# Kernel tuning notes

Hardware: AMD Instinct MI355X
Metric: run time of the kernel (lower is better)

Reference implementation:

```python
import jax, jax.numpy as jnp
import numpy as np

NUM_HEADS = 16
D_MODEL = 1024
D_K = D_MODEL // NUM_HEADS


def setup_inputs() -> dict:
    key = jax.random.key(0)
    ks = jax.random.split(key, 12)
    B, S = 2, 2048
    scale = 1.0 / np.sqrt(D_MODEL)
    inp = {
        "query": jax.random.normal(ks[0], (B, S, D_MODEL), jnp.float32),
        "key": jax.random.normal(ks[1], (B, S, D_MODEL), jnp.float32),
        "value": jax.random.normal(ks[2], (B, S, D_MODEL), jnp.float32),
        "mask": jnp.ones((B, S, S), jnp.int32),
        "Wq": jax.random.normal(ks[3], (D_MODEL, D_MODEL), jnp.float32) * scale,
        "bq": jax.random.normal(ks[4], (D_MODEL,), jnp.float32) * scale,
        "Wk": jax.random.normal(ks[5], (D_MODEL, D_MODEL), jnp.float32) * scale,
        "bk": jax.random.normal(ks[6], (D_MODEL,), jnp.float32) * scale,
        "Wv": jax.random.normal(ks[7], (D_MODEL, D_MODEL), jnp.float32) * scale,
        "bv": jax.random.normal(ks[8], (D_MODEL,), jnp.float32) * scale,
        "Wo": jax.random.normal(ks[9], (D_MODEL, D_MODEL), jnp.float32) * scale,
        "bo": jax.random.normal(ks[10], (D_MODEL,), jnp.float32) * scale,
    }
    return inp


def _split_heads(x):
    B, S, _ = x.shape
    return x.reshape(B, S, NUM_HEADS, D_K).transpose(0, 2, 1, 3)  # [B,H,S,d_k]


def reference(query, key, value, mask, Wq, bq, Wk, bk, Wv, bv, Wo, bo):
    # torch Linear: y = x @ W.T + b
    q = _split_heads(query @ Wq.T + bq)
    k = _split_heads(key @ Wk.T + bk)
    v = _split_heads(value @ Wv.T + bv)
    scores = jnp.einsum("bhqd,bhkd->bhqk", q, k) / np.sqrt(D_K)
    scores = jnp.where(mask[:, None, :, :] == 0, jnp.float32(-1e9), scores)
    p_attn = jax.nn.softmax(scores, axis=-1)
    attn = jnp.einsum("bhqk,bhkd->bhqd", p_attn, v)  # [B,H,S,d_k]
    B, _, S, _ = attn.shape
    x = attn.transpose(0, 2, 1, 3).reshape(B, S, D_MODEL)
    return x @ Wo.T + bo
```

## Files before the change

kernel.cpp:

```cpp
#include <hip/hip_runtime.h>
#include <hip/hip_bf16.h>
#include <cstdint>

#define DEVINL static __device__ __forceinline__

typedef __attribute__((ext_vector_type(4))) float floatx4;
typedef __attribute__((ext_vector_type(8))) short bf16x8;

DEVINL unsigned short f2bf(float f) {
    union { float f; uint32_t u; } v; v.f = f;
    return (unsigned short)((v.u + 0x7FFFu + ((v.u >> 16) & 1u)) >> 16);
}

DEVINL uint32_t pk2bf(float x, float y) {
    __hip_bfloat162 h = __float22bfloat162_rn(float2{x, y});
    union { __hip_bfloat162 h; uint32_t u; } v; v.h = h;
    return v.u;
}

DEVINL floatx4 mfma16(bf16x8 a, bf16x8 b, floatx4 c) {
    return __builtin_amdgcn_mfma_f32_16x16x32_bf16(a, b, c, 0, 0, 0);
}

#define GLDS16(g, l)                                                            \
    __builtin_amdgcn_global_load_lds(                                           \
        (const __attribute__((address_space(1))) void*)(g),                     \
        (__attribute__((address_space(3))) void*)(l), 16, 0, 0)

constexpr int B_ = 2, S_ = 2048, D_ = 1024, H_ = 16, DK_ = 64;
constexpr int BSROWS = B_ * S_;
constexpr int NQB = S_ / 128;
constexpr int NKT = S_ / 64;

constexpr float QSCALE = 0.18033688011112042f;

__device__ int g_flags[B_ * NQB * NKT];

__global__ __launch_bounds__(256, 2)
void gemm_qkv(const float* __restrict__ q, const float* __restrict__ k,
              const float* __restrict__ v,
              const float* __restrict__ Wq, const float* __restrict__ Wk,
              const float* __restrict__ Wv,
              const float* __restrict__ bq, const float* __restrict__ bk,
              const float* __restrict__ bv,
              const int* __restrict__ mask,
              unsigned short* __restrict__ Qp, unsigned short* __restrict__ KpF,
              unsigned short* __restrict__ VpF)
{
    constexpr int K = D_, N = D_;
    __shared__ unsigned short As[2][128 * 64];
    __shared__ unsigned short Bs[2][128 * 64];
    __shared__ int fflag;

    const int bid = blockIdx.x;

    if (bid < 1024) {
        int mb = bid;
        int kt = mb & 31, qq = (mb >> 5) & 15, b = mb >> 9;
        const int* base = mask + (size_t)(b * S_ + qq * 128) * S_ + kt * 64;
        int ok = 1;
        #pragma unroll
        for (int i = 0; i < 8; ++i) {
            int u = threadIdx.x + 256 * i;
            int row = u >> 4, c = u & 15;
            int4 m = *(const int4*)(base + (size_t)row * S_ + c * 4);
            if ((m.x == 0) | (m.y == 0) | (m.z == 0) | (m.w == 0)) ok = 0;
        }
        if (threadIdx.x == 0) fflag = 1;
        __syncthreads();
        if (!ok) fflag = 0;
        __syncthreads();
        if (threadIdx.x == 0) g_flags[mb] = fflag;
        return;
    }

    const int gb = bid - 1024;
    const int xcd = gb & 7, sl = gb >> 3;
    const int z = sl >> 5, rr = sl & 31;
    const int nb = rr >> 2, mloc = rr & 3;
    const int m0 = (mloc * 8 + xcd) * 128, n0 = nb * 128;

    const float* A    = z == 0 ? q  : z == 1 ? k  : v;
    const float* W    = z == 0 ? Wq : z == 1 ? Wk : Wv;
    const float* bias = z == 0 ? bq : z == 1 ? bk : bv;

    const int tid  = threadIdx.x;
    const int lane = tid & 63, wave = tid >> 6;
    const int lr = lane & 15, lg = lane >> 4;
    const int wm = (wave >> 1) * 64, wn = (wave & 1) * 64;

    int rowA[4], kcA[4];
    #pragma unroll
    for (int j = 0; j < 4; ++j) {
        int L = (wave * 4 + j) * 64 + lane;
        rowA[j] = L >> 3; kcA[j] = (L & 7) ^ (rowA[j] & 7);
    }

    float4 ra[4][2], rw[4][2];
    auto loadStage = [&](int k0) {
        #pragma unroll
        for (int j = 0; j < 4; ++j) {
            const float* pa = A + (size_t)(m0 + rowA[j]) * K + k0 + kcA[j] * 8;
            ra[j][0] = *(const float4*)pa;
            ra[j][1] = *(const float4*)(pa + 4);
            const float* pw = W + (size_t)(n0 + rowA[j]) * K + k0 + kcA[j] * 8;
            rw[j][0] = *(const float4*)pw;
            rw[j][1] = *(const float4*)(pw + 4);
        }
    };
    auto writeStage = [&](int buf) {
        #pragma unroll
        for (int j = 0; j < 4; ++j) {
            uint4 o;
            o.x = pk2bf(ra[j][0].x, ra[j][0].y); o.y = pk2bf(ra[j][0].z, ra[j][0].w);
            o.z = pk2bf(ra[j][1].x, ra[j][1].y); o.w = pk2bf(ra[j][1].z, ra[j][1].w);
            *(uint4*)&As[buf][(wave * 4 + j) * 512 + lane * 8] = o;
            uint4 p;
            p.x = pk2bf(rw[j][0].x, rw[j][0].y); p.y = pk2bf(rw[j][0].z, rw[j][0].w);
            p.z = pk2bf(rw[j][1].x, rw[j][1].y); p.w = pk2bf(rw[j][1].z, rw[j][1].w);
            *(uint4*)&Bs[buf][(wave * 4 + j) * 512 + lane * 8] = p;
        }
    };

    floatx4 acc[4][4];
    #pragma unroll
    for (int mt = 0; mt < 4; ++mt)
        #pragma unroll
        for (int nt = 0; nt < 4; ++nt)
            acc[mt][nt] = floatx4{0.f, 0.f, 0.f, 0.f};

    loadStage(0);
    writeStage(0);
    __syncthreads();
    for (int it = 0; it < K / 64; ++it) {
        const int buf = it & 1;
        if (it + 1 < K / 64) loadStage((it + 1) * 64);

        #pragma unroll
        for (int kf = 0; kf < 2; ++kf) {
            bf16x8 af[4], bfr[4];
            #pragma unroll
            for (int mt = 0; mt < 4; ++mt) {
                int row = wm + mt * 16 + lr;
                af[mt] = *(const bf16x8*)&As[buf][row * 64 + (((kf * 4 + lg) ^ (lr & 7)) * 8)];
            }
            #pragma unroll
            for (int nt = 0; nt < 4; ++nt) {
                int row = wn + nt * 16 + lr;
                bfr[nt] = *(const bf16x8*)&Bs[buf][row * 64 + (((kf * 4 + lg) ^ (lr & 7)) * 8)];
            }
            #pragma unroll
            for (int mt = 0; mt < 4; ++mt)
                #pragma unroll
                for (int nt = 0; nt < 4; ++nt)
                    acc[mt][nt] = mfma16(af[mt], bfr[nt], acc[mt][nt]);
        }

        if (it + 1 < K / 64) writeStage(buf ^ 1);
        __syncthreads();
    }

    if (z == 0) {
        #pragma unroll
        for (int nt = 0; nt < 4; ++nt) {
            int col = n0 + wn + nt * 16 + lr;
            float bv2 = bias[col];
            #pragma unroll
            for (int mt = 0; mt < 4; ++mt)
                #pragma unroll
                for (int reg = 0; reg < 4; ++reg) {
                    int row = m0 + wm + mt * 16 + lg * 4 + reg;
                    Qp[(size_t)row * N + col] = f2bf((acc[mt][nt][reg] + bv2) * QSCALE);
                }
        }
    } else if (z == 1) {
        #pragma unroll
        for (int nt = 0; nt < 4; ++nt) {
            int c = n0 + wn + nt * 16 + lr;
            int h = c >> 6, d = c & 63;
            int kfA = d >> 5, lgA = (d >> 3) & 3, j = d & 7;
            float bv2 = bias[c];
            #pragma unroll
            for (int mt = 0; mt < 4; ++mt)
                #pragma unroll
                for (int reg = 0; reg < 4; ++reg) {
                    int t = m0 + wm + mt * 16 + lg * 4 + reg;
                    int bb = t >> 11, sx = t & (S_ - 1);
                    int kt = sx >> 6, key = sx & 63;
                    int mtA = key >> 4, lrA = key & 15;
                    size_t off = (((size_t)(bb * 16 + h) * 32 + kt) * 8 + (kfA * 4 + mtA)) * 512
                               + (lrA + 16 * lgA) * 8 + j;
                    KpF[off] = f2bf(acc[mt][nt][reg] + bv2);
                }
        }
    } else {
        #pragma unroll
        for (int nt = 0; nt < 4; ++nt) {
            int c = n0 + wn + nt * 16 + lr;
            int h = c >> 6, dtA = (c >> 4) & 3;
            float bv2 = bias[c];
            #pragma unroll
            for (int mt = 0; mt < 4; ++mt) {
                int t0 = m0 + wm + mt * 16 + lg * 4;
                int bb = t0 >> 11, s0 = t0 & (S_ - 1);
                int kt = s0 >> 6, key = s0 & 63;
                int kfA = key >> 5, lgA = (key >> 3) & 3, j0 = key & 7;
                size_t off = (((size_t)(bb * 16 + h) * 32 + kt) * 8 + (dtA * 2 + kfA)) * 512
                           + (lr + 16 * lgA) * 8 + j0;
                uint2 p;
                p.x = pk2bf(acc[mt][nt][0] + bv2, acc[mt][nt][1] + bv2);
                p.y = pk2bf(acc[mt][nt][2] + bv2, acc[mt][nt][3] + bv2);
                *(uint2*)&VpF[off] = p;
            }
        }
    }
}

__global__ __launch_bounds__(256, 2)
void attn_flash(const unsigned short* __restrict__ Qp,
                const unsigned short* __restrict__ KpF,
                const unsigned short* __restrict__ VpF,
                const int* __restrict__ mask,
                unsigned short* __restrict__ Out)
{
    constexpr int LD = 72;
    __shared__ unsigned short Ps[128 * LD];

    const int tid = threadIdx.x;
    const int lane = tid & 63, wave = tid >> 6;
    const int lr = lane & 15, lg = lane >> 4;
    const int id = blockIdx.x;
    const int hb = id & 31;
    const int h = hb & 15, b = hb >> 4;
    const int qb = ((id >> 8) << 3) | ((id >> 5) & 7);
    const int q0 = qb * 128, qw = q0 + wave * 32;

    bf16x8 qf[2][2];
    #pragma unroll
    for (int qt = 0; qt < 2; ++qt)
        #pragma unroll
        for (int kf = 0; kf < 2; ++kf)
            qf[qt][kf] = *(const bf16x8*)(Qp + (size_t)(b * S_ + qw + qt * 16 + lr) * D_ +
                                          h * DK_ + kf * 32 + lg * 8);

    float l_[2] = {0.f, 0.f};
    floatx4 o_acc[2][4];
    #pragma unroll
    for (int qt = 0; qt < 2; ++qt)
        #pragma unroll
        for (int dt = 0; dt < 4; ++dt) o_acc[qt][dt] = floatx4{0.f, 0.f, 0.f, 0.f};

    const unsigned short* kbase = KpF + (size_t)(b * 16 + h) * 32 * 4096 + lane * 8;
    const unsigned short* vbase = VpF + (size_t)(b * 16 + h) * 32 * 4096 + lane * 8;
    const int fbase = (b * NQB + qb) * NKT;
    unsigned short* PsW = &Ps[(wave * 32 + lr) * LD];

    auto loadKV = [&](int kt, bf16x8 (&kfr)[8], bf16x8 (&vfr)[8]) {
        const unsigned short* kb = kbase + kt * 4096;
        const unsigned short* vb = vbase + kt * 4096;
        #pragma unroll
        for (int c = 0; c < 8; ++c) kfr[c] = *(const bf16x8*)(kb + c * 512);
        #pragma unroll
        for (int c = 0; c < 8; ++c) vfr[c] = *(const bf16x8*)(vb + c * 512);
    };

    auto process = [&](int kt, bf16x8 (&kfr)[8], bf16x8 (&vfr)[8]) {
        floatx4 sc[2][4];
        #pragma unroll
        for (int qt = 0; qt < 2; ++qt)
            #pragma unroll
            for (int mt = 0; mt < 4; ++mt) sc[qt][mt] = floatx4{0.f, 0.f, 0.f, 0.f};
        #pragma unroll
        for (int mt = 0; mt < 4; ++mt)
            #pragma unroll
            for (int kf = 0; kf < 2; ++kf)
                #pragma unroll
                for (int qt = 0; qt < 2; ++qt)
                    sc[qt][mt] = mfma16(kfr[kf * 4 + mt], qf[qt][kf], sc[qt][mt]);

        if (g_flags[fbase + kt] == 0) {
            #pragma unroll
            for (int qt = 0; qt < 2; ++qt) {
                int qq = qw + qt * 16 + lr;
                const int* mrow = mask + (size_t)(b * S_ + qq) * S_ + kt * 64;
                #pragma unroll
                for (int mt = 0; mt < 4; ++mt)
                    #pragma unroll
                    for (int reg = 0; reg < 4; ++reg)
                        if (mrow[mt * 16 + lg * 4 + reg] == 0)
                            sc[qt][mt][reg] = -1e9f;
            }
        }

        #pragma unroll
        for (int qt = 0; qt < 2; ++qt) {
            #pragma unroll
            for (int mt = 0; mt < 4; ++mt) {
                float p0 = __builtin_amdgcn_exp2f(sc[qt][mt][0]);
                float p1 = __builtin_amdgcn_exp2f(sc[qt][mt][1]);
                float p2 = __builtin_amdgcn_exp2f(sc[qt][mt][2]);
                float p3 = __builtin_amdgcn_exp2f(sc[qt][mt][3]);
                l_[qt] += (p0 + p1) + (p2 + p3);
                uint2 pk; pk.x = pk2bf(p0, p1); pk.y = pk2bf(p2, p3);
                *(uint2*)&PsW[qt * 16 * LD + mt * 16 + lg * 4] = pk;
            }
        }

        bf16x8 pb[2][2];
        #pragma unroll
        for (int qt = 0; qt < 2; ++qt)
            #pragma unroll
            for (int kf = 0; kf < 2; ++kf)
                pb[qt][kf] = *(const bf16x8*)&PsW[qt * 16 * LD + kf * 32 + lg * 8];
        #pragma unroll
        for (int dt = 0; dt < 4; ++dt)
            #pragma unroll
            for (int kf = 0; kf < 2; ++kf)
                #pragma unroll
                for (int qt = 0; qt < 2; ++qt)
                    o_acc[qt][dt] = mfma16(vfr[dt * 2 + kf], pb[qt][kf], o_acc[qt][dt]);
    };

    bf16x8 kA[8], vA[8], kB[8], vB[8];
    loadKV(0, kA, vA);
    for (int kt = 0; kt < NKT; kt += 2) {
        loadKV(kt + 1, kB, vB);
        process(kt, kA, vA);
        if (kt + 2 < NKT) loadKV(kt + 2, kA, vA);
        process(kt + 1, kB, vB);
    }

    #pragma unroll
    for (int qt = 0; qt < 2; ++qt) {
        float l = l_[qt];
        l += __shfl_xor(l, 16, 64);
        l += __shfl_xor(l, 32, 64);
        float inv = 1.f / l;
        int qq = qw + qt * 16 + lr;
        #pragma unroll
        for (int dt = 0; dt < 4; ++dt) {
            uint2 p;
            p.x = pk2bf(o_acc[qt][dt][0] * inv, o_acc[qt][dt][1] * inv);
            p.y = pk2bf(o_acc[qt][dt][2] * inv, o_acc[qt][dt][3] * inv);
            *(uint2*)&Out[(size_t)(b * S_ + qq) * D_ + h * DK_ + dt * 16 + lg * 4] = p;
        }
    }
}

__global__ __launch_bounds__(256)
void gemm_out(const unsigned short* __restrict__ Ap,
              const float* __restrict__ Wo,
              const float* __restrict__ bias, float* __restrict__ Cptr)
{
    constexpr int K = D_, N = D_;
    __shared__ unsigned short As[2][128 * 64];
    __shared__ unsigned short Wss[2][64 * 64];

    const int bid = blockIdx.x;
    const int xcd = bid & 7, sl = bid >> 3;
    const int nb = sl >> 2, mloc = sl & 3;
    const int m0 = (mloc * 8 + xcd) * 128, n0 = nb * 64;

    const int tid  = threadIdx.x;
    const int lane = tid & 63, wave = tid >> 6;
    const int lr = lane & 15, lg = lane >> 4;
    const int wm = (wave >> 1) * 64, wn = (wave & 1) * 32;

    int rowA[4], kcA[4], rowW[2], kcW[2];
    #pragma unroll
    for (int j = 0; j < 4; ++j) {
        int L = (wave * 4 + j) * 64 + lane;
        rowA[j] = L >> 3; kcA[j] = (L & 7) ^ (rowA[j] & 7);
    }
    #pragma unroll
    for (int j = 0; j < 2; ++j) {
        int L = (wave * 2 + j) * 64 + lane;
        rowW[j] = L >> 3; kcW[j] = (L & 7) ^ (rowW[j] & 7);
    }

    auto dmaA = [&](int k0, int buf) {
        #pragma unroll
        for (int j = 0; j < 4; ++j)
            GLDS16(Ap + (size_t)(m0 + rowA[j]) * K + k0 + kcA[j] * 8,
                   &As[buf][(wave * 4 + j) * 512 + lane * 8]);
    };

    float4 rw[2][2];
    auto loadW = [&](int k0) {
        #pragma unroll
        for (int j = 0; j < 2; ++j) {
            const float* pw = Wo + (size_t)(n0 + rowW[j]) * K + k0 + kcW[j] * 8;
            rw[j][0] = *(const float4*)pw;
            rw[j][1] = *(const float4*)(pw + 4);
        }
    };
    auto writeW = [&](int buf) {
        #pragma unroll
        for (int j = 0; j < 2; ++j) {
            uint4 p;
            p.x = pk2bf(rw[j][0].x, rw[j][0].y); p.y = pk2bf(rw[j][0].z, rw[j][0].w);
            p.z = pk2bf(rw[j][1].x, rw[j][1].y); p.w = pk2bf(rw[j][1].z, rw[j][1].w);
            *(uint4*)&Wss[buf][(wave * 2 + j) * 512 + lane * 8] = p;
        }
    };

    floatx4 acc[4][2];
    #pragma unroll
    for (int mt = 0; mt < 4; ++mt)
        #pragma unroll
        for (int nt = 0; nt < 2; ++nt)
            acc[mt][nt] = floatx4{0.f, 0.f, 0.f, 0.f};

    dmaA(0, 0);
    loadW(0); writeW(0);
    __syncthreads();
    for (int it = 0; it < K / 64; ++it) {
        const int buf = it & 1;
        if (it + 1 < K / 64) { dmaA((it + 1) * 64, buf ^ 1); loadW((it + 1) * 64); }

        #pragma unroll
        for (int kf = 0; kf < 2; ++kf) {
            bf16x8 af[4], bfr[2];
            #pragma unroll
            for (int mt = 0; mt < 4; ++mt) {
                int row = wm + mt * 16 + lr;
                af[mt] = *(const bf16x8*)&As[buf][row * 64 + (((kf * 4 + lg) ^ (lr & 7)) * 8)];
            }
            #pragma unroll
            for (int nt = 0; nt < 2; ++nt) {
                int row = wn + nt * 16 + lr;
                bfr[nt] = *(const bf16x8*)&Wss[buf][row * 64 + (((kf * 4 + lg) ^ (lr & 7)) * 8)];
            }
            #pragma unroll
            for (int mt = 0; mt < 4; ++mt)
                #pragma unroll
                for (int nt = 0; nt < 2; ++nt)
                    acc[mt][nt] = mfma16(af[mt], bfr[nt], acc[mt][nt]);
        }

        if (it + 1 < K / 64) writeW(buf ^ 1);
        __syncthreads();
    }

    #pragma unroll
    for (int nt = 0; nt < 2; ++nt) {
        int col = n0 + wn + nt * 16 + lr;
        float bv2 = bias[col];
        #pragma unroll
        for (int mt = 0; mt < 4; ++mt)
            #pragma unroll
            for (int reg = 0; reg < 4; ++reg) {
                int row = m0 + wm + mt * 16 + lg * 4 + reg;
                Cptr[(size_t)row * N + col] = acc[mt][nt][reg] + bv2;
            }
    }
}

extern "C" void kernel_launch(void* const* d_in, const int* in_sizes, int n_in,
                              void* d_out, int out_size, void* d_ws, size_t ws_size,
                              hipStream_t stream)
{
    const float* query = (const float*)d_in[0];
    const float* key   = (const float*)d_in[1];
    const float* value = (const float*)d_in[2];
    const int*   mask  = (const int*)d_in[3];
    const float* Wq = (const float*)d_in[4];
    const float* bq = (const float*)d_in[5];
    const float* Wk = (const float*)d_in[6];
    const float* bk = (const float*)d_in[7];
    const float* Wv = (const float*)d_in[8];
    const float* bv = (const float*)d_in[9];
    const float* Wo = (const float*)d_in[10];
    const float* bo = (const float*)d_in[11];

    unsigned short* Qp  = (unsigned short*)d_ws;
    unsigned short* KpF = Qp  + (size_t)BSROWS * D_;
    unsigned short* VpF = KpF + (size_t)BSROWS * D_;
    unsigned short* Ap  = VpF + (size_t)BSROWS * D_;

    dim3 blk(256);

    hipLaunchKernelGGL(gemm_qkv, dim3(1024 + 768), blk, 0, stream,
                       query, key, value, Wq, Wk, Wv, bq, bk, bv, mask,
                       Qp, KpF, VpF);

    hipLaunchKernelGGL(attn_flash, dim3(512), blk, 0, stream, Qp, KpF, VpF, mask, Ap);

    hipLaunchKernelGGL(gemm_out, dim3(512), blk, 0, stream, Ap, Wo, bo, (float*)d_out);
}
```

Baseline: 272.9 us.

## Deepen register prefetch to two stages and stage Q/K epilogue through LDS

The QKV projection and output GEMM loops now load global data two iterations ahead and write the previously loaded registers to LDS at the start of each iteration, instead of after compute. This aims to hide global load latency behind a full iteration of MFMA work. The Q and K epilogues also stage results in shared memory and then write coalesced 16-byte vectors, replacing scattered 2-byte stores. The cost is higher register pressure from holding prefetched data across the compute phase, plus an extra barrier in the epilogue.

Result: faster. 255.2 us (-6.5%).

```diff
diff --git a/kernel.cpp b/kernel.cpp
--- a/kernel.cpp
+++ b/kernel.cpp
@@ -131,10 +131,12 @@
 
     loadStage(0);
     writeStage(0);
+    loadStage(64);
     __syncthreads();
     for (int it = 0; it < K / 64; ++it) {
         const int buf = it & 1;
-        if (it + 1 < K / 64) loadStage((it + 1) * 64);
+        if (it + 1 < K / 64) writeStage(buf ^ 1);
+        if (it + 2 < K / 64) loadStage((it + 2) * 64);
 
         #pragma unroll
         for (int kf = 0; kf < 2; ++kf) {
@@ -155,43 +157,58 @@
                 for (int nt = 0; nt < 4; ++nt)
                     acc[mt][nt] = mfma16(af[mt], bfr[nt], acc[mt][nt]);
         }
-
-        if (it + 1 < K / 64) writeStage(buf ^ 1);
         __syncthreads();
     }
 
+    unsigned short* Cs = &As[0][0];
+
     if (z == 0) {
         #pragma unroll
         for (int nt = 0; nt < 4; ++nt) {
-            int col = n0 + wn + nt * 16 + lr;
-            float bv2 = bias[col];
+            int cl = wn + nt * 16 + lr;
+            float bv2 = bias[n0 + cl];
             #pragma unroll
             for (int mt = 0; mt < 4; ++mt)
                 #pragma unroll
                 for (int reg = 0; reg < 4; ++reg) {
-                    int row = m0 + wm + mt * 16 + lg * 4 + reg;
-                    Qp[(size_t)row * N + col] = f2bf((acc[mt][nt][reg] + bv2) * QSCALE);
+                    int rl = wm + mt * 16 + lg * 4 + reg;
+                    Cs[rl * 128 + cl] = f2bf((acc[mt][nt][reg] + bv2) * QSCALE);
                 }
         }
+        __syncthreads();
+        #pragma unroll
+        for (int i = 0; i < 8; ++i) {
+            int e = tid * 8 + i;
+            int rl = e >> 4, cc = (e & 15) * 8;
+            *(uint4*)&Qp[(size_t)(m0 + rl) * N + n0 + cc] = *(uint4*)&Cs[e * 8];
+        }
     } else if (z == 1) {
+        const int bb = m0 >> 11, kt0 = (m0 & 2047) >> 6, h0 = n0 >> 6;
         #pragma unroll
         for (int nt = 0; nt < 4; ++nt) {
-            int c = n0 + wn + nt * 16 + lr;
-            int h = c >> 6, d = c & 63;
+            int cl = wn + nt * 16 + lr;
+            int hh = cl >> 6, d = cl & 63;
             int kfA = d >> 5, lgA = (d >> 3) & 3, j = d & 7;
-            float bv2 = bias[c];
+            float bv2 = bias[n0 + cl];
             #pragma unroll
             for (int mt = 0; mt < 4; ++mt)
                 #pragma unroll
                 for (int reg = 0; reg < 4; ++reg) {
-                    int t = m0 + wm + mt * 16 + lg * 4 + reg;
-                    int bb = t >> 11, sx = t & (S_ - 1);
-                    int kt = sx >> 6, key = sx & 63;
+                    int tl = wm + mt * 16 + lg * 4 + reg;
+                    int tt = tl >> 6, key = tl & 63;
                     int mtA = key >> 4, lrA = key & 15;
-                    size_t off = (((size_t)(bb * 16 + h) * 32 + kt) * 8 + (kfA * 4 + mtA)) * 512
-                               + (lrA + 16 * lgA) * 8 + j;
-                    KpF[off] = f2bf(acc[mt][nt][reg] + bv2);
+                    Cs[(hh * 2 + tt) * 4096 + (kfA * 4 + mtA) * 512 +
+                       (lrA + 16 * lgA) * 8 + j] = f2bf(acc[mt][nt][reg] + bv2);
                 }
+        }
+        __syncthreads();
+        #pragma unroll
+        for (int i = 0; i < 8; ++i) {
+            int e = tid * 8 + i;
+            int s = e >> 9, w = e & 511;
+            int hh = s >> 1, tt = s & 1;
+            size_t gbase = (((size_t)(bb * 16 + h0 + hh)) * 32 + (kt0 + tt)) * 4096;
+            *(uint4*)&KpF[gbase + w * 8] = *(uint4*)&Cs[e * 8];
         }
     } else {
         #pragma unroll
@@ -412,11 +429,12 @@
             acc[mt][nt] = floatx4{0.f, 0.f, 0.f, 0.f};
 
     dmaA(0, 0);
-    loadW(0); writeW(0);
+    loadW(0); writeW(0); loadW(64);
     __syncthreads();
     for (int it = 0; it < K / 64; ++it) {
         const int buf = it & 1;
-        if (it + 1 < K / 64) { dmaA((it + 1) * 64, buf ^ 1); loadW((it + 1) * 64); }
+        if (it + 1 < K / 64) { dmaA((it + 1) * 64, buf ^ 1); writeW(buf ^ 1); }
+        if (it + 2 < K / 64) loadW((it + 2) * 64);
 
         #pragma unroll
         for (int kf = 0; kf < 2; ++kf) {
@@ -437,8 +455,6 @@
                 for (int nt = 0; nt < 2; ++nt)
                     acc[mt][nt] = mfma16(af[mt], bfr[nt], acc[mt][nt]);
         }
-
-        if (it + 1 < K / 64) writeW(buf ^ 1);
         __syncthreads();
     }
 
```
